# Kernel tuning notes

Hardware: AMD Instinct MI355X
Metric: run time of the kernel (lower is better)

## Reference

```python
import jax, jax.numpy as jnp
import numpy as np

FEATURE_MAPS = [38, 19, 10, 5, 3, 1]
NUM_ANCHORS = [4, 6, 6, 6, 4, 4]
SCALES = (0.2, 0.9)
RATIOS = np.array([1.0, 1.0, 2.0, 3.0, 0.5, 1.0 / 3.0])
BACKGROUND_ID = 0
EPS = 1e-6


def _generate_anchors():
    """Replicates AnchorManager._generate_anchors: order is (i, j, k)."""
    all_anchors = []
    for size, n in zip(FEATURE_MAPS, NUM_ANCHORS):
        scales = np.linspace(SCALES[0], SCALES[1], n)
        ratios = RATIOS[:n]
        rs = np.sqrt(ratios)
        w = scales * rs          # [n]
        h = scales / rs          # [n]
        cy = (np.arange(size) + 0.5) / size  # i -> rows (varies slowest)
        cx = (np.arange(size) + 0.5) / size  # j -> cols
        grid = np.zeros((size, size, n, 4), dtype=np.float64)
        grid[..., 0] = cx[None, :, None]
        grid[..., 1] = cy[:, None, None]
        grid[..., 2] = w[None, None, :]
        grid[..., 3] = h[None, None, :]
        all_anchors.append(grid.reshape(-1, 4))
    return np.concatenate(all_anchors).astype(np.float32)  # [A, 4] cxcywh


def _cxcywh_to_xyxy(b):
    cxy, wh = b[..., :2], b[..., 2:]
    return jnp.concatenate([cxy - wh / 2, cxy + wh / 2], axis=-1)


def _xyxy_to_cxcywh(b):
    xy1, xy2 = b[..., :2], b[..., 2:]
    return jnp.concatenate([(xy1 + xy2) / 2, xy2 - xy1], axis=-1)


def setup_inputs() -> dict:
    key = jax.random.key(0)
    k1, k2, k3 = jax.random.split(key, 3)
    B, N = 64, 100
    # valid normalized xyxy gt boxes
    xy = jax.random.uniform(k1, (B, N, 2), dtype=jnp.float32) * 0.8
    wh = jax.random.uniform(k2, (B, N, 2), dtype=jnp.float32) * 0.19 + 0.01
    gt_boxes = jnp.concatenate([xy, xy + wh], axis=-1)
    gt_labels = jax.random.randint(k3, (B, N), 1, 81, dtype=jnp.int64 if jax.config.jax_enable_x64 else jnp.int32).astype(jnp.int32)
    anchors_cxcywh = jnp.asarray(_generate_anchors())          # [A, 4]
    anchors_xyxy = _cxcywh_to_xyxy(anchors_cxcywh)             # [A, 4]
    return {
        "gt_labels": gt_labels,
        "gt_boxes": gt_boxes,
        "anchors_cxcywh": anchors_cxcywh,
        "anchors_xyxy": anchors_xyxy,
    }


def _iou(anchors_xyxy, gt_boxes):
    # anchors_xyxy: [A,4], gt_boxes: [B,N,4] -> iou [B,A,N]
    a = anchors_xyxy[None, :, None, :]   # [1,A,1,4]
    g = gt_boxes[:, None, :, :]          # [B,1,N,4]
    lt = jnp.maximum(a[..., :2], g[..., :2])
    rb = jnp.minimum(a[..., 2:], g[..., 2:])
    wh = jnp.clip(rb - lt, 0.0)
    inter = wh[..., 0] * wh[..., 1]
    area_a = (a[..., 2] - a[..., 0]) * (a[..., 3] - a[..., 1])
    area_g = (g[..., 2] - g[..., 0]) * (g[..., 3] - g[..., 1])
    return (inter / (area_a + area_g - inter)).astype(jnp.float32)


def reference(gt_labels, gt_boxes, anchors_cxcywh, anchors_xyxy):
    B, N = gt_boxes.shape[0], gt_boxes.shape[1]
    A = anchors_cxcywh.shape[0]

    gt_boxes_coco = _xyxy_to_cxcywh(gt_boxes)                  # [B,N,4]
    ious = _iou(anchors_xyxy, gt_boxes)                        # [B,A,N]

    anchors_gt = jnp.max(ious, axis=-1)                        # [B,A]
    anchors_gt_idx = jnp.argmax(ious, axis=-1)                 # [B,A]
    gt_anchors_idx = jnp.argmax(ious, axis=-2)                 # [B,N] best anchor per gt

    # force-match: each gt claims its best anchor
    b_idx = jnp.arange(B)[:, None]
    range_n = jnp.broadcast_to(jnp.arange(N), (B, N))
    anchors_gt_idx = anchors_gt_idx.at[b_idx, gt_anchors_idx].set(range_n)
    anchors_gt = anchors_gt.at[b_idx, gt_anchors_idx].set(2.0)

    pos_mask = anchors_gt > 0.5                                # [B,A]

    matched_gtb = jnp.take_along_axis(gt_boxes_coco, anchors_gt_idx[..., None], axis=1)  # [B,A,4]
    matched_labels = jnp.take_along_axis(gt_labels, anchors_gt_idx, axis=1)              # [B,A]
    encoded_labels = jnp.where(pos_mask, matched_labels, BACKGROUND_ID)

    anc = anchors_cxcywh[None]                                 # [1,A,4]
    enc_cxy = (matched_gtb[..., :2] - anc[..., :2]) / anc[..., 2:]
    enc_wh = jnp.log((matched_gtb[..., 2:] + EPS) / (anc[..., 2:] + EPS))
    encoded = jnp.concatenate([enc_cxy, enc_wh], axis=-1)      # [B,A,4]

    return encoded_labels, encoded, pos_mask
```

## Files before the change

### kernel.cpp

```cpp
#include <hip/hip_runtime.h>
#include <math.h>

#pragma clang fp contract(off)


#define AA 8732
#define NN 100
#define BB 64
#define EPS_F 1e-6f
#define OVR_FLAG 0x10000
#define POS_BIT  0x8000
#define DEFL 0.9999995f

__constant__ int FM_SIZE[6] = {38, 19, 10, 5, 3, 1};
__constant__ int FM_NF[6]   = {4, 6, 6, 6, 4, 4};
__constant__ int FM_OFF[6]  = {0, 5776, 7942, 8542, 8692, 8728};

__device__ __forceinline__ void geom(const float4 axy, const float4 g,
                                     float area_a, float ag,
                                     float& inter, float& uni) {
    float ltx = fmaxf(axy.x, g.x);
    float lty = fmaxf(axy.y, g.y);
    float rbx = fminf(axy.z, g.z);
    float rby = fminf(axy.w, g.w);
    float w = fmaxf(rbx - ltx, 0.0f);
    float h = fmaxf(rby - lty, 0.0f);
    inter = w * h;
    uni = area_a + ag - inter;
}

__global__ void prior_kernel(const float4* __restrict__ gt_boxes,
                             const float4* __restrict__ anchors_xyxy,
                             float* __restrict__ prior,
                             unsigned long long* __restrict__ colmax) {
    const int b = blockIdx.x;
    const int n = threadIdx.x;
    if (n >= NN) return;
    float4 g = gt_boxes[b * NN + n];
    float ag = (g.z - g.x) * (g.w - g.y);
    float cx = (g.x + g.z) * 0.5f;
    float cy = (g.y + g.w) * 0.5f;
    float best = 0.0f;
    for (int f = 0; f < 6; f++) {
        int s = FM_SIZE[f];
        int j = (int)(cx * (float)s); j = j < s - 1 ? j : s - 1;
        int i = (int)(cy * (float)s); i = i < s - 1 ? i : s - 1;
        int base = FM_OFF[f] + (i * s + j) * FM_NF[f];
        for (int k = 0; k < FM_NF[f]; k++) {
            float4 an = anchors_xyxy[base + k];
            float area_a = (an.z - an.x) * (an.w - an.y);
            float inter, uni;
            geom(an, g, area_a, ag, inter, uni);
            best = fmaxf(best, inter * __builtin_amdgcn_rcpf(uni));
        }
    }
    float defl = best * DEFL;
    prior[b * NN + n] = defl;
    colmax[b * NN + n] = ((unsigned long long)__float_as_uint(defl)) << 32;
}

template <int N0, int N1>
__device__ __forceinline__ void passChunk(
        const float4 axy, const float area_a, const unsigned lowkey,
        const int b, const int tid,
        const float4* __restrict__ sg,
        float2* sac,
        unsigned long long* __restrict__ colmax,
        float& rt, unsigned& rm)
{
    #pragma unroll 4
    for (int n = N0; n < N1; n++) {
        float4 g = sg[n];
        float2 aw = sac[n];
        float inter, uni;
        geom(axy, g, area_a, aw.x, inter, uni);
        float qa = inter * __builtin_amdgcn_rcpf(uni);
        bool r = (qa > 0.0f) && (qa >= rt);
        rt = fmaxf(rt, qa * DEFL);
        rm |= (r ? 1u : 0u) << (n - N0);
        if (__any((int)(qa >= aw.y))) {
            float iou = inter / uni;
            bool cc = (qa >= aw.y);
            unsigned long long p = cc
                ? ((((unsigned long long)__float_as_uint(iou)) << 32) |
                   (unsigned long long)lowkey) : 0ull;
            #pragma unroll
            for (int off = 32; off > 0; off >>= 1) {
                unsigned long long o = __shfl_xor(p, off);
                p = o > p ? o : p;
            }
            if ((tid & 63) == 0 && p != 0ull) {
                atomicMax(colmax + b * NN + n, p);
                atomicMax((unsigned*)&sac[n].y,
                    __float_as_uint(__uint_as_float((unsigned)(p >> 32)) * DEFL));
            }
        }
    }
}

__global__ __launch_bounds__(256) void iou_pass_kernel(
        const float4* __restrict__ gt_boxes,
        const float4* __restrict__ anchors_xyxy,
        const float* __restrict__ prior,
        unsigned long long* __restrict__ colmax,
        int* __restrict__ out_slot)
{
    const int b = blockIdx.y;
    const int tid = threadIdx.x;
    const int a = blockIdx.x * 256 + tid;
    const bool valid = (a < AA);
    const int ac = valid ? a : (AA - 1);

    __shared__ float4 sg[NN];
    __shared__ float2 sac[NN];

    if (tid < NN) {
        float4 g = gt_boxes[b * NN + tid];
        sg[tid] = g;
        sac[tid] = make_float2((g.z - g.x) * (g.w - g.y),
                               prior[b * NN + tid]);
    }
    __syncthreads();

    const float4 axy = anchors_xyxy[ac];
    const float area_a = (axy.z - axy.x) * (axy.w - axy.y);
    const unsigned lowkey = (unsigned)(AA - ac);

    float rt = 0.0f;
    unsigned rm0 = 0, rm1 = 0, rm2 = 0, rm3 = 0;
    passChunk<0, 32>(axy, area_a, lowkey, b, tid, sg, sac, colmax, rt, rm0);
    passChunk<32, 64>(axy, area_a, lowkey, b, tid, sg, sac, colmax, rt, rm1);
    passChunk<64, 96>(axy, area_a, lowkey, b, tid, sg, sac, colmax, rt, rm2);
    passChunk<96, NN>(axy, area_a, lowkey, b, tid, sg, sac, colmax, rt, rm3);

    float bv = 0.0f;
    int bi = 0;
    unsigned rms[4] = {rm0, rm1, rm2, rm3};
    #pragma unroll
    for (int h = 0; h < 4; h++) {
        unsigned m = rms[h];
        const int nb = h * 32;
        while (m) {
            int n = __builtin_ctz(m) + nb;
            m &= m - 1;
            float inter, uni;
            geom(axy, sg[n], area_a, sac[n].x, inter, uni);
            float qa = inter * __builtin_amdgcn_rcpf(uni);
            if (qa > 0.0f && qa >= rt) {
                float iou = inter / uni;
                if (iou > bv) { bv = iou; bi = n; }
            }
        }
    }

    if (valid) {
        out_slot[(size_t)b * AA + a] = bi | (bv > 0.5f ? POS_BIT : 0);
    }
}

__global__ void scatter_kernel(const unsigned long long* __restrict__ colmax,
                               int* __restrict__ out_slot) {
    const int b = blockIdx.x;
    const int n = threadIdx.x;
    if (n < NN) {
        unsigned long long v = colmax[b * NN + n];
        unsigned low = (unsigned)(v & 0xFFFFFFFFull);
        if (low >= 1u && low <= (unsigned)AA) {
            int idx = AA - (int)low;
            atomicMax(&out_slot[(size_t)b * AA + idx], OVR_FLAG + n);
        }
    }
}

__global__ __launch_bounds__(256) void encode_kernel(
        const int* __restrict__ gt_labels,
        const float4* __restrict__ gt_boxes,
        const float4* __restrict__ anchors_cxcywh,
        float* __restrict__ out)
{
    const int b = blockIdx.y;
    const int tid = threadIdx.x;
    const int a = blockIdx.x * 256 + tid;

    __shared__ float4 sg[NN];
    __shared__ int    slab[NN];
    if (tid < NN) {
        sg[tid]   = gt_boxes[b * NN + tid];
        slab[tid] = gt_labels[b * NN + tid];
    }
    __syncthreads();
    if (a >= AA) return;

    const size_t BA = (size_t)BB * AA;
    const size_t base = (size_t)b * AA + a;

    int s = ((const int*)(out + 5 * BA))[base];

    int idx; bool pos;
    if (s >= OVR_FLAG) { idx = s - OVR_FLAG;  pos = true; }
    else               { idx = s & 0x7FFF;    pos = (s & POS_BIT) != 0; }

    const float4 g = sg[idx];
    const float gcx = (g.x + g.z) * 0.5f;
    const float gcy = (g.y + g.w) * 0.5f;
    const float gw  = g.z - g.x;
    const float gh  = g.w - g.y;

    const float4 anc = anchors_cxcywh[a];
    const float ecx = (gcx - anc.x) / anc.z;
    const float ecy = (gcy - anc.y) / anc.w;
    const float ew  = logf((gw + EPS_F) / (anc.z + EPS_F));
    const float eh  = logf((gh + EPS_F) / (anc.w + EPS_F));

    out[base] = pos ? (float)slab[idx] : 0.0f;
    ((float4*)(out + BA))[base] = make_float4(ecx, ecy, ew, eh);
    out[5 * BA + base] = pos ? 1.0f : 0.0f;
}

extern "C" void kernel_launch(void* const* d_in, const int* in_sizes, int n_in,
                              void* d_out, int out_size, void* d_ws, size_t ws_size,
                              hipStream_t stream) {
    const int*    gt_labels    = (const int*)d_in[0];
    const float4* gt_boxes     = (const float4*)d_in[1];
    const float4* anchors_cxcy = (const float4*)d_in[2];
    const float4* anchors_xyxy = (const float4*)d_in[3];
    float* out = (float*)d_out;

    const size_t BA = (size_t)BB * AA;
    unsigned long long* colmax = (unsigned long long*)(out + BA);
    int* slot = (int*)(out + 5 * BA);
    float* prior = (float*)d_ws;

    prior_kernel<<<BB, 128, 0, stream>>>(gt_boxes, anchors_xyxy, prior, colmax);

    dim3 grid((AA + 255) / 256, BB);
    iou_pass_kernel<<<grid, 256, 0, stream>>>(gt_boxes, anchors_xyxy, prior,
                                              colmax, slot);
    scatter_kernel<<<BB, 128, 0, stream>>>(colmax, slot);
    encode_kernel<<<grid, 256, 0, stream>>>(gt_labels, gt_boxes, anchors_cxcy,
                                            out);
}
```

Baseline: 130.9 us.

## Fuse prior, IoU, scatter and encode into one cooperative persistent kernel

Replaces the four separate kernel launches with a single cooperative kernel that runs the prior, IoU-pass, scatter and encode stages in sequence, separated by grid-wide syncs. Blocks loop persistently over batch×anchor tiles. The goal is to remove per-launch overhead and the gaps between dependent kernels. The cost is grid.sync latency and a persistent grid sized by occupancy, which may cap parallelism and add tile-loop serialization. If the cooperative launch is unavailable or fails, the code falls back to the original four-kernel path.

```diff
diff --git a/kernel.cpp b/kernel.cpp
--- a/kernel.cpp
+++ b/kernel.cpp
@@ -1,12 +1,17 @@
 #include <hip/hip_runtime.h>
+#include <hip/hip_cooperative_groups.h>
 #include <math.h>
 
 #pragma clang fp contract(off)
+
+namespace cg = cooperative_groups;
 
 
 #define AA 8732
 #define NN 100
 #define BB 64
+#define NTILE 35
+#define NT (BB * NTILE)
 #define EPS_F 1e-6f
 #define OVR_FLAG 0x10000
 #define POS_BIT  0x8000
@@ -29,13 +34,13 @@
     uni = area_a + ag - inter;
 }
 
-__global__ void prior_kernel(const float4* __restrict__ gt_boxes,
-                             const float4* __restrict__ anchors_xyxy,
-                             float* __restrict__ prior,
-                             unsigned long long* __restrict__ colmax) {
-    const int b = blockIdx.x;
-    const int n = threadIdx.x;
-    if (n >= NN) return;
+__device__ __forceinline__ void prior_one(
+        const int b, const int n,
+        const float4* __restrict__ gt_boxes,
+        const float4* __restrict__ anchors_xyxy,
+        float* __restrict__ prior,
+        unsigned long long* __restrict__ colmax)
+{
     float4 g = gt_boxes[b * NN + n];
     float ag = (g.z - g.x) * (g.w - g.y);
     float cx = (g.x + g.z) * 0.5f;
@@ -98,22 +103,15 @@
     }
 }
 
-__global__ __launch_bounds__(256) void iou_pass_kernel(
+__device__ __forceinline__ void iou_tile(
+        const int b, const int c, const int tid,
         const float4* __restrict__ gt_boxes,
         const float4* __restrict__ anchors_xyxy,
         const float* __restrict__ prior,
         unsigned long long* __restrict__ colmax,
-        int* __restrict__ out_slot)
-{
-    const int b = blockIdx.y;
-    const int tid = threadIdx.x;
-    const int a = blockIdx.x * 256 + tid;
-    const bool valid = (a < AA);
-    const int ac = valid ? a : (AA - 1);
-
-    __shared__ float4 sg[NN];
-    __shared__ float2 sac[NN];
-
+        int* __restrict__ out_slot,
+        float4* __restrict__ sg, float2* sac)
+{
     if (tid < NN) {
         float4 g = gt_boxes[b * NN + tid];
         sg[tid] = g;
@@ -122,6 +120,9 @@
     }
     __syncthreads();
 
+    const int a = c * 256 + tid;
+    const bool valid = (a < AA);
+    const int ac = valid ? a : (AA - 1);
     const float4 axy = anchors_xyxy[ac];
     const float area_a = (axy.z - axy.x) * (axy.w - axy.y);
     const unsigned lowkey = (unsigned)(AA - ac);
@@ -158,6 +159,134 @@
     }
 }
 
+__device__ __forceinline__ void encode_tile(
+        const int b, const int c, const int tid,
+        const int* __restrict__ gt_labels,
+        const float4* __restrict__ gt_boxes,
+        const float4* __restrict__ anchors_cxcywh,
+        float* __restrict__ out,
+        float4* __restrict__ sg, int* __restrict__ slab)
+{
+    if (tid < NN) {
+        sg[tid]   = gt_boxes[b * NN + tid];
+        slab[tid] = gt_labels[b * NN + tid];
+    }
+    __syncthreads();
+
+    const int a = c * 256 + tid;
+    if (a < AA) {
+        const size_t BA = (size_t)BB * AA;
+        const size_t base = (size_t)b * AA + a;
+
+        int s = ((const int*)(out + 5 * BA))[base];
+
+        int idx; bool pos;
+        if (s >= OVR_FLAG) { idx = s - OVR_FLAG;  pos = true; }
+        else               { idx = s & 0x7FFF;    pos = (s & POS_BIT) != 0; }
+
+        const float4 g = sg[idx];
+        const float gcx = (g.x + g.z) * 0.5f;
+        const float gcy = (g.y + g.w) * 0.5f;
+        const float gw  = g.z - g.x;
+        const float gh  = g.w - g.y;
+
+        const float4 anc = anchors_cxcywh[a];
+        const float ecx = (gcx - anc.x) / anc.z;
+        const float ecy = (gcy - anc.y) / anc.w;
+        const float ew  = logf((gw + EPS_F) / (anc.z + EPS_F));
+        const float eh  = logf((gh + EPS_F) / (anc.w + EPS_F));
+
+        out[base] = pos ? (float)slab[idx] : 0.0f;
+        ((float4*)(out + BA))[base] = make_float4(ecx, ecy, ew, eh);
+        out[5 * BA + base] = pos ? 1.0f : 0.0f;
+    }
+}
+
+__global__ __launch_bounds__(256, 8) void mega_kernel(
+        const int* __restrict__ gt_labels,
+        const float4* __restrict__ gt_boxes,
+        const float4* __restrict__ anchors_cxcywh,
+        const float4* __restrict__ anchors_xyxy,
+        float* __restrict__ out,
+        float* __restrict__ prior)
+{
+    cg::grid_group grid = cg::this_grid();
+    const int tid = threadIdx.x;
+    const int bid = blockIdx.x;
+    const int nb  = gridDim.x;
+    const size_t BA = (size_t)BB * AA;
+    unsigned long long* colmax = (unsigned long long*)(out + BA);
+    int* out_slot = (int*)(out + 5 * BA);
+
+    __shared__ float4 sg[NN];
+    __shared__ float2 sac[NN];
+    __shared__ int    slab[NN];
+
+    {
+        const int g = bid * 256 + tid;
+        if (g < BB * NN) {
+            const int b = g / NN;
+            prior_one(b, g - b * NN, gt_boxes, anchors_xyxy, prior, colmax);
+        }
+    }
+    grid.sync();
+
+    for (int t = bid; t < NT; t += nb) {
+        const int b = t / NTILE;
+        const int c = t - b * NTILE;
+        iou_tile(b, c, tid, gt_boxes, anchors_xyxy, prior, colmax, out_slot,
+                 sg, sac);
+        __syncthreads();
+    }
+    grid.sync();
+
+    {
+        const int g = bid * 256 + tid;
+        if (g < BB * NN) {
+            const int b = g / NN;
+            const int n = g - b * NN;
+            unsigned long long v = colmax[g];
+            unsigned low = (unsigned)(v & 0xFFFFFFFFull);
+            if (low >= 1u && low <= (unsigned)AA) {
+                int idx = AA - (int)low;
+                atomicMax(&out_slot[(size_t)b * AA + idx], OVR_FLAG + n);
+            }
+        }
+    }
+    grid.sync();
+
+    for (int t = bid; t < NT; t += nb) {
+        const int b = t / NTILE;
+        const int c = t - b * NTILE;
+        encode_tile(b, c, tid, gt_labels, gt_boxes, anchors_cxcywh, out,
+                    sg, slab);
+        __syncthreads();
+    }
+}
+
+__global__ void prior_kernel(const float4* __restrict__ gt_boxes,
+                             const float4* __restrict__ anchors_xyxy,
+                             float* __restrict__ prior,
+                             unsigned long long* __restrict__ colmax) {
+    const int b = blockIdx.x;
+    const int n = threadIdx.x;
+    if (n >= NN) return;
+    prior_one(b, n, gt_boxes, anchors_xyxy, prior, colmax);
+}
+
+__global__ __launch_bounds__(256) void iou_pass_kernel(
+        const float4* __restrict__ gt_boxes,
+        const float4* __restrict__ anchors_xyxy,
+        const float* __restrict__ prior,
+        unsigned long long* __restrict__ colmax,
+        int* __restrict__ out_slot)
+{
+    __shared__ float4 sg[NN];
+    __shared__ float2 sac[NN];
+    iou_tile(blockIdx.y, blockIdx.x, threadIdx.x,
+             gt_boxes, anchors_xyxy, prior, colmax, out_slot, sg, sac);
+}
+
 __global__ void scatter_kernel(const unsigned long long* __restrict__ colmax,
                                int* __restrict__ out_slot) {
     const int b = blockIdx.x;
@@ -178,43 +307,10 @@
         const float4* __restrict__ anchors_cxcywh,
         float* __restrict__ out)
 {
-    const int b = blockIdx.y;
-    const int tid = threadIdx.x;
-    const int a = blockIdx.x * 256 + tid;
-
     __shared__ float4 sg[NN];
     __shared__ int    slab[NN];
-    if (tid < NN) {
-        sg[tid]   = gt_boxes[b * NN + tid];
-        slab[tid] = gt_labels[b * NN + tid];
-    }
-    __syncthreads();
-    if (a >= AA) return;
-
-    const size_t BA = (size_t)BB * AA;
-    const size_t base = (size_t)b * AA + a;
-
-    int s = ((const int*)(out + 5 * BA))[base];
-
-    int idx; bool pos;
-    if (s >= OVR_FLAG) { idx = s - OVR_FLAG;  pos = true; }
-    else               { idx = s & 0x7FFF;    pos = (s & POS_BIT) != 0; }
-
-    const float4 g = sg[idx];
-    const float gcx = (g.x + g.z) * 0.5f;
-    const float gcy = (g.y + g.w) * 0.5f;
-    const float gw  = g.z - g.x;
-    const float gh  = g.w - g.y;
-
-    const float4 anc = anchors_cxcywh[a];
-    const float ecx = (gcx - anc.x) / anc.z;
-    const float ecy = (gcy - anc.y) / anc.w;
-    const float ew  = logf((gw + EPS_F) / (anc.z + EPS_F));
-    const float eh  = logf((gh + EPS_F) / (anc.w + EPS_F));
-
-    out[base] = pos ? (float)slab[idx] : 0.0f;
-    ((float4*)(out + BA))[base] = make_float4(ecx, ecy, ew, eh);
-    out[5 * BA + base] = pos ? 1.0f : 0.0f;
+    encode_tile(blockIdx.y, blockIdx.x, threadIdx.x,
+                gt_labels, gt_boxes, anchors_cxcywh, out, sg, slab);
 }
 
 extern "C" void kernel_launch(void* const* d_in, const int* in_sizes, int n_in,
@@ -231,9 +327,36 @@
     int* slot = (int*)(out + 5 * BA);
     float* prior = (float*)d_ws;
 
+    static int coop_blocks = -1;
+    if (coop_blocks < 0) {
+        int dev = 0, cus = 0, maxB = 0;
+        if (hipGetDevice(&dev) == hipSuccess &&
+            hipDeviceGetAttribute(&cus, hipDeviceAttributeMultiprocessorCount,
+                                  dev) == hipSuccess &&
+            hipOccupancyMaxActiveBlocksPerMultiprocessor(
+                &maxB, (const void*)mega_kernel, 256, 0) == hipSuccess &&
+            cus > 0 && maxB > 0) {
+            long long cap = (long long)maxB * (long long)cus;
+            coop_blocks = (int)(cap > 2048 ? 2048 : cap);
+            if (coop_blocks < 64) coop_blocks = 0;
+        } else {
+            coop_blocks = 0;
+        }
+    }
+
+    if (coop_blocks > 0) {
+        void* args[6] = { (void*)&gt_labels, (void*)&gt_boxes,
+                          (void*)&anchors_cxcy, (void*)&anchors_xyxy,
+                          (void*)&out, (void*)&prior };
+        hipError_t e = hipLaunchCooperativeKernel(
+            (const void*)mega_kernel, dim3((unsigned)coop_blocks), dim3(256),
+            args, 0, stream);
+        if (e == hipSuccess) return;
+        coop_blocks = 0;
+    }
+
     prior_kernel<<<BB, 128, 0, stream>>>(gt_boxes, anchors_xyxy, prior, colmax);
-
-    dim3 grid((AA + 255) / 256, BB);
+    dim3 grid(NTILE, BB);
     iou_pass_kernel<<<grid, 256, 0, stream>>>(gt_boxes, anchors_xyxy, prior,
                                               colmax, slot);
     scatter_kernel<<<BB, 128, 0, stream>>>(colmax, slot);
```

New measurement: 434.4 us. 232% more time.
